# Performance work log

Measured on AMD Instinct MI355X. Metric: run time of the kernel, lower is better.

Reference implementation:

```python
import jax, jax.numpy as jnp
import numpy as np

N_WIRES = 12
BLOCK_CONFIGS = [(12, 3), (12, 3)]
HAM_OFFSET = 0.0
HAM_COEFF = 1.0
BATCH = 4096


def _sq(psi, w):
    # view statevector (B, 2^n) as (B, left, 2, right) isolating wire w
    B = psi.shape[0]
    n = N_WIRES
    return psi.reshape(B, 1 << w, 2, 1 << (n - 1 - w))


def _rx(psi, theta, w):
    s = _sq(psi, w)
    t = jnp.asarray(theta, jnp.float32).reshape(-1, 1, 1, 1) * 0.5
    out = jnp.cos(t) * s - 1j * jnp.sin(t) * jnp.flip(s, axis=2)
    return out.reshape(psi.shape)


def _ry(psi, theta, w):
    # [[c,-s],[s,c]]: new = cos*psi + sin*sgn*flip(psi), sgn = (-1, +1)
    s = _sq(psi, w)
    t = jnp.asarray(theta, jnp.float32).reshape(-1, 1, 1, 1) * 0.5
    sgn = jnp.array([-1.0, 1.0], jnp.float32).reshape(1, 1, 2, 1)
    out = jnp.cos(t) * s + jnp.sin(t) * sgn * jnp.flip(s, axis=2)
    return out.reshape(psi.shape)


def _rz(psi, theta, w):
    # diag(e^{-i t/2}, e^{+i t/2})
    s = _sq(psi, w)
    t = jnp.asarray(theta, jnp.float32).reshape(-1, 1, 1, 1) * 0.5
    z = jnp.array([-1.0, 1.0], jnp.float32).reshape(1, 1, 2, 1)
    out = s * jnp.exp(1j * (t * z).astype(jnp.complex64))
    return out.reshape(psi.shape)


def _cnot(psi, c, t):
    B = psi.shape[0]
    n = N_WIRES
    lo, hi = (c, t) if c < t else (t, c)
    s = psi.reshape(B, 1 << lo, 2, 1 << (hi - lo - 1), 2, 1 << (n - 1 - hi))
    ctrl_ax = 2 if c == lo else 4
    tgt_ax = 4 if c == lo else 2
    p0 = jax.lax.index_in_dim(s, 0, axis=ctrl_ax, keepdims=True)
    p1 = jnp.flip(jax.lax.index_in_dim(s, 1, axis=ctrl_ax, keepdims=True), axis=tgt_ax)
    out = jnp.concatenate([p0, p1], axis=ctrl_ax)
    return out.reshape(psi.shape)


def setup_inputs() -> dict:
    key = jax.random.key(0)
    k1, k2 = jax.random.split(key)
    total_encode = sum(ne for ne, _ in BLOCK_CONFIGS)
    total_ansatz = sum(ld for _, ld in BLOCK_CONFIGS)
    x = jax.random.normal(k1, (BATCH, total_encode), dtype=jnp.float32)
    ansatz_weights = jax.random.uniform(
        k2, (total_ansatz, 3, N_WIRES), dtype=jnp.float32,
        minval=-np.pi, maxval=np.pi)
    return {"x": x, "ansatz_weights": ansatz_weights}


def reference(x, ansatz_weights):
    B = x.shape[0]
    n = N_WIRES
    psi = jnp.zeros((B, 1 << n), jnp.complex64).at[:, 0].set(1.0)
    param_col = 0
    ansatz_block = 0
    for n_encode, linear_depth in BLOCK_CONFIGS:
        for j in range(n_encode):
            wire = j % n
            if param_col < x.shape[1]:
                psi = _rx(psi, x[:, param_col], wire)
            param_col += 1
        for _ in range(linear_depth):
            w = ansatz_weights[ansatz_block]
            for i in range(n):
                psi = _ry(psi, w[0, i], i)
                psi = _rz(psi, w[1, i], i)
                psi = _ry(psi, w[2, i], i)
            for i in range(n):
                psi = _cnot(psi, i, (i + 1) % n)
            ansatz_block += 1
    # <H> with H = offset + coeff * sum_i Z_i : diagonal = n - 2*popcount(k)
    probs = psi.real ** 2 + psi.imag ** 2
    k = jnp.arange(1 << n)
    pop = ((k[:, None] >> jnp.arange(n)[None, :]) & 1).sum(-1).astype(jnp.float32)
    diag = HAM_OFFSET + HAM_COEFF * (n - 2.0 * pop)
    expval = probs @ diag  # (B,)
    return expval[:, None]
```

## Files before the change

### kernel.cpp

```cpp
#include <hip/hip_runtime.h>
#include <math.h>

#define NT 256
#define NS 4096

typedef float f32x2 __attribute__((ext_vector_type(2)));

constexpr int ring_pi_c(int k) {
    int u = k ^ (k >> 1);
    u ^= u >> 2; u ^= u >> 4; u ^= u >> 8;
    int w0 = ((u >> 11) ^ u) & 1;
    return (u & 0x7FF) | (w0 << 11);
}
constexpr int sig2(int m) { return m ^ ((m >> 4) & 0xF) ^ ((m >> 8) & 0xF); }

__device__ __forceinline__ void app1p(f32x2 ab, f32x2 cd, f32x2& a0, f32x2& a1) {
    f32x2 n0, n1;
    asm("v_pk_mul_f32 %0, %2, %4 op_sel:[0,0] op_sel_hi:[1,0]\n\t"
        "v_pk_fma_f32 %0, %2, %4, %0 op_sel:[1,1,0] op_sel_hi:[0,1,1] neg_hi:[0,1,0]\n\t"
        "v_pk_fma_f32 %0, %3, %5, %0 op_sel:[0,0,0] op_sel_hi:[1,0,1] neg_lo:[0,1,0] neg_hi:[0,1,0]\n\t"
        "v_pk_fma_f32 %0, %3, %5, %0 op_sel:[1,1,0] op_sel_hi:[0,1,1] neg_lo:[0,1,0]\n\t"
        "v_pk_mul_f32 %1, %3, %4 op_sel:[0,0] op_sel_hi:[1,0]\n\t"
        "v_pk_fma_f32 %1, %3, %4, %1 op_sel:[1,1,0] op_sel_hi:[0,1,1] neg_lo:[0,1,0]\n\t"
        "v_pk_fma_f32 %1, %2, %5, %1 op_sel:[0,0,0] op_sel_hi:[1,0,1]\n\t"
        "v_pk_fma_f32 %1, %2, %5, %1 op_sel:[1,1,0] op_sel_hi:[0,1,1] neg_lo:[0,1,0]"
        : "=&v"(n0), "=&v"(n1)
        : "v"(a0), "v"(a1), "v"(ab), "v"(cd));
    a0 = n0; a1 = n1;
}

template<int P>
__device__ __forceinline__ void gate_on_bit(f32x2 a[16], f32x2 ab, f32x2 cd) {
    #pragma unroll
    for (int r = 0; r < 16; ++r)
        if (!(r & (1 << P)))
            app1p(ab, cd, a[r], a[r | (1 << P)]);
}

__device__ __forceinline__ void load_gate(const float4* __restrict__ Uw,
                                          const float2* __restrict__ cs12,
                                          int l, int w, bool fold,
                                          f32x2& ab, f32x2& cd) {
    float4 g = Uw[l * 12 + w];
    float A = g.x, B = g.y, C = g.z, D = g.w;
    if (fold) {
        float2 sc = cs12[w];
        float c = sc.x, s = sc.y;
        float A2 = A*c + D*s, B2 = B*c - C*s, C2 = C*c + B*s, D2 = D*c - A*s;
        A = A2; B = B2; C = C2; D = D2;
    }
    ab = f32x2{A, B}; cd = f32x2{C, D};
}

__global__ void prep_kernel(const float* __restrict__ x,
                            const float* __restrict__ wts,
                            float4* __restrict__ Uw,
                            float2* __restrict__ cs,
                            int total)
{
    int idx = blockIdx.x * blockDim.x + threadIdx.x;
    if (idx < total) {
        float th = 0.5f * x[idx];
        float s, c; sincosf(th, &s, &c);
        cs[idx] = make_float2(c, s);
    }
    if (idx < 72) {
        int ab = idx / 12, w = idx % 12;
        float a  = 0.5f * wts[(ab * 3 + 0) * 12 + w];
        float bb = 0.5f * wts[(ab * 3 + 1) * 12 + w];
        float g  = 0.5f * wts[(ab * 3 + 2) * 12 + w];
        float sa, ca, sb, cb, sg, cg;
        sincosf(a,  &sa, &ca);
        sincosf(bb, &sb, &cb);
        sincosf(g,  &sg, &cg);
        float A = cb * (ca * cg - sa * sg);
        float B = sb * (ca * cg + sa * sg);
        float C = cb * (sa * cg + ca * sg);
        float D = sb * (sa * cg - ca * sg);
        Uw[idx] = make_float4(A, B, C, D);
    }
}

__global__ __launch_bounds__(NT, 2)
void tqhea_kernel(const float4* __restrict__ Uw,
                  const float2* __restrict__ cs,
                  float* __restrict__ out)
{
    __shared__ f32x2 psi[NS];

    const int b = blockIdx.x;
    const int t = threadIdx.x;

    const int lo = t & 0xF, h = t >> 4;
    const int tb     = (t & 0xF0) | (lo ^ h);
    const int baseP1 = (h << 8) | (lo ^ h);
    const int baseP2 = (t << 4) | (lo ^ h);
    const int Qt     = sig2(ring_pi_c(t << 4));
    const int Pt     = ring_pi_c(t << 4);

    const float2* csb  = cs + b * 24;
    const float2* cs12 = csb + 12;

    {
        float2 rc[12];
        #pragma unroll
        for (int i = 0; i < 12; ++i) rc[i] = csb[i];
        float mlo = 1.f;
        #pragma unroll
        for (int bit = 0; bit < 8; ++bit)
            mlo *= ((t >> bit) & 1) ? rc[11 - bit].y : rc[11 - bit].x;
        int pct = __popc(t);
        #pragma unroll
        for (int r = 0; r < 16; ++r) {
            float mhi = 1.f;
            #pragma unroll
            for (int p = 0; p < 4; ++p)
                mhi *= ((r >> p) & 1) ? rc[3 - p].y : rc[3 - p].x;
            float mag = mhi * mlo;
            int pc = (pct + __popc(r)) & 3;
            f32x2 v;
            v.x = (pc == 0) ? mag : ((pc == 2) ? -mag : 0.f);
            v.y = (pc == 1) ? -mag : ((pc == 3) ? mag : 0.f);
            psi[(r << 8) | (tb ^ r)] = v;
        }
    }
    __syncthreads();

    float acc = 0.f;

    #pragma unroll 1
    for (int l = 0; l < 6; ++l) {
        const bool fold = (l == 3);
        f32x2 a[16];
        f32x2 gab, gcd;

        #pragma unroll
        for (int r = 0; r < 16; ++r) a[r] = psi[(r << 8) | (tb ^ r)];
        load_gate(Uw, cs12, l, 0, fold, gab, gcd); gate_on_bit<3>(a, gab, gcd);
        load_gate(Uw, cs12, l, 1, fold, gab, gcd); gate_on_bit<2>(a, gab, gcd);
        load_gate(Uw, cs12, l, 2, fold, gab, gcd); gate_on_bit<1>(a, gab, gcd);
        load_gate(Uw, cs12, l, 3, fold, gab, gcd); gate_on_bit<0>(a, gab, gcd);
        #pragma unroll
        for (int r = 0; r < 16; ++r) psi[(r << 8) | (tb ^ r)] = a[r];
        __syncthreads();

        #pragma unroll
        for (int r = 0; r < 16; ++r) a[r] = psi[baseP1 ^ (17 * r)];
        load_gate(Uw, cs12, l, 4, fold, gab, gcd); gate_on_bit<3>(a, gab, gcd);
        load_gate(Uw, cs12, l, 5, fold, gab, gcd); gate_on_bit<2>(a, gab, gcd);
        load_gate(Uw, cs12, l, 6, fold, gab, gcd); gate_on_bit<1>(a, gab, gcd);
        load_gate(Uw, cs12, l, 7, fold, gab, gcd); gate_on_bit<0>(a, gab, gcd);
        #pragma unroll
        for (int r = 0; r < 16; ++r) psi[baseP1 ^ (17 * r)] = a[r];
        __syncthreads();

        #pragma unroll
        for (int r = 0; r < 16; ++r) a[r] = psi[baseP2 ^ r];
        if (l < 5) __syncthreads();
        load_gate(Uw, cs12, l, 8,  fold, gab, gcd); gate_on_bit<3>(a, gab, gcd);
        load_gate(Uw, cs12, l, 9,  fold, gab, gcd); gate_on_bit<2>(a, gab, gcd);
        load_gate(Uw, cs12, l, 10, fold, gab, gcd); gate_on_bit<1>(a, gab, gcd);
        load_gate(Uw, cs12, l, 11, fold, gab, gcd); gate_on_bit<0>(a, gab, gcd);
        if (l < 5) {
            #pragma unroll
            for (int r = 0; r < 16; ++r)
                psi[Qt ^ sig2(ring_pi_c(r))] = a[r];
            __syncthreads();
        } else {
            #pragma unroll
            for (int r = 0; r < 16; ++r) {
                float d = 12.0f - 2.0f * (float)__popc(Pt ^ ring_pi_c(r));
                acc += (a[r].x * a[r].x + a[r].y * a[r].y) * d;
            }
        }
    }

    #pragma unroll
    for (int off = 32; off > 0; off >>= 1)
        acc += __shfl_down(acc, off);
    __syncthreads();
    if ((t & 63) == 0) ((float*)psi)[t >> 6] = acc;
    __syncthreads();
    if (t == 0) {
        const float* rb = (const float*)psi;
        out[b] = rb[0] + rb[1] + rb[2] + rb[3];
    }
}

extern "C" void kernel_launch(void* const* d_in, const int* in_sizes, int n_in,
                              void* d_out, int out_size, void* d_ws, size_t ws_size,
                              hipStream_t stream) {
    const float* x   = (const float*)d_in[0];
    const float* wts = (const float*)d_in[1];
    float* out = (float*)d_out;
    int B = in_sizes[0] / 24;

    float4* Uw = (float4*)d_ws;
    float2* cs = (float2*)((char*)d_ws + 1152);
    int total = B * 24;

    prep_kernel<<<dim3((total + NT - 1) / NT), dim3(NT), 0, stream>>>(x, wts, Uw, cs, total);
    tqhea_kernel<<<dim3(B), dim3(NT), 0, stream>>>(Uw, cs, out);
}
```

Measured before the change: 215.4 us.

## Simulate each statevector with one 64-lane wavefront holding 64 amplitudes per lane

The batch kernel now uses a single 64-thread wavefront per sample instead of 256 threads. Each lane keeps 64 complex amplitudes in registers, so six gates are applied per register pass and only two LDS transposes are needed per layer instead of three. The initial encoded state is built directly in registers, and the final reduction becomes a single wave shuffle. In exchange, register pressure rises sharply (128 floats of state per lane), which risks spills, and the number of waves per CU drops.

```diff
diff --git a/kernel.cpp b/kernel.cpp
--- a/kernel.cpp
+++ b/kernel.cpp
@@ -1,7 +1,8 @@
 #include <hip/hip_runtime.h>
 #include <math.h>
 
-#define NT 256
+#define NTP 256
+#define NT 64
 #define NS 4096
 
 typedef float f32x2 __attribute__((ext_vector_type(2)));
@@ -12,7 +13,11 @@
     int w0 = ((u >> 11) ^ u) & 1;
     return (u & 0x7FF) | (w0 << 11);
 }
-constexpr int sig2(int m) { return m ^ ((m >> 4) & 0xF) ^ ((m >> 8) & 0xF); }
+constexpr int gfun(int n) {
+    int n0 = n & 1, n1 = (n >> 1) & 1, n2 = (n >> 2) & 1, n3 = (n >> 3) & 1;
+    return (n1) | ((n0 ^ n1 ^ n2) << 1) | ((n0 ^ n2 ^ n3) << 2) | ((n0 ^ n3) << 3);
+}
+constexpr int sigf(int k) { return k ^ gfun((k >> 6) & 15); }
 
 __device__ __forceinline__ void app1p(f32x2 ab, f32x2 cd, f32x2& a0, f32x2& a1) {
     f32x2 n0, n1;
@@ -30,18 +35,18 @@
 }
 
 template<int P>
-__device__ __forceinline__ void gate_on_bit(f32x2 a[16], f32x2 ab, f32x2 cd) {
+__device__ __forceinline__ void gate_on_bit6(f32x2 a[64], f32x2 ab, f32x2 cd) {
     #pragma unroll
-    for (int r = 0; r < 16; ++r)
+    for (int r = 0; r < 64; ++r)
         if (!(r & (1 << P)))
             app1p(ab, cd, a[r], a[r | (1 << P)]);
 }
 
 __device__ __forceinline__ void load_gate(const float4* __restrict__ Uw,
                                           const float2* __restrict__ cs12,
-                                          int l, int w, bool fold,
+                                          int lay, int w, bool fold,
                                           f32x2& ab, f32x2& cd) {
-    float4 g = Uw[l * 12 + w];
+    float4 g = Uw[lay * 12 + w];
     float A = g.x, B = g.y, C = g.z, D = g.w;
     if (fold) {
         float2 sc = cs12[w];
@@ -81,95 +86,97 @@
     }
 }
 
-__global__ __launch_bounds__(NT, 2)
+__global__ __launch_bounds__(NT, 1)
 void tqhea_kernel(const float4* __restrict__ Uw,
                   const float2* __restrict__ cs,
                   float* __restrict__ out)
 {
     __shared__ f32x2 psi[NS];
 
-    const int b = blockIdx.x;
-    const int t = threadIdx.x;
-
-    const int lo = t & 0xF, h = t >> 4;
-    const int tb     = (t & 0xF0) | (lo ^ h);
-    const int baseP1 = (h << 8) | (lo ^ h);
-    const int baseP2 = (t << 4) | (lo ^ h);
-    const int Qt     = sig2(ring_pi_c(t << 4));
-    const int Pt     = ring_pi_c(t << 4);
+    const int b  = blockIdx.x;
+    const int ln = threadIdx.x;
 
     const float2* csb  = cs + b * 24;
     const float2* cs12 = csb + 12;
 
+    f32x2 a[64];
+
     {
         float2 rc[12];
         #pragma unroll
         for (int i = 0; i < 12; ++i) rc[i] = csb[i];
-        float mlo = 1.f;
-        #pragma unroll
-        for (int bit = 0; bit < 8; ++bit)
-            mlo *= ((t >> bit) & 1) ? rc[11 - bit].y : rc[11 - bit].x;
-        int pct = __popc(t);
-        #pragma unroll
-        for (int r = 0; r < 16; ++r) {
-            float mhi = 1.f;
+        float mlan = 1.f;
+        #pragma unroll
+        for (int bit = 0; bit < 6; ++bit)
+            mlan *= ((ln >> bit) & 1) ? rc[11 - bit].y : rc[11 - bit].x;
+        int q = __popc(ln) & 3;
+        float pre = (q == 0) ? mlan : (q == 2) ? -mlan : 0.f;
+        float pim = (q == 1) ? -mlan : (q == 3) ? mlan : 0.f;
+        float mA[8], mB[8];
+        #pragma unroll
+        for (int i = 0; i < 8; ++i) {
+            mA[i] = (((i>>2)&1)?rc[0].y:rc[0].x) * (((i>>1)&1)?rc[1].y:rc[1].x) * ((i&1)?rc[2].y:rc[2].x);
+            mB[i] = (((i>>2)&1)?rc[3].y:rc[3].x) * (((i>>1)&1)?rc[4].y:rc[4].x) * ((i&1)?rc[5].y:rc[5].x);
+        }
+        #pragma unroll
+        for (int r = 0; r < 64; ++r) {
+            float m = mA[r >> 3] * mB[r & 7];
+            const int rot = __popc(r) & 3;
+            float vx, vy;
+            if (rot == 0)      { vx =  pre * m; vy =  pim * m; }
+            else if (rot == 1) { vx =  pim * m; vy = -pre * m; }
+            else if (rot == 2) { vx = -pre * m; vy = -pim * m; }
+            else               { vx = -pim * m; vy =  pre * m; }
+            a[r] = f32x2{vx, vy};
+        }
+    }
+
+    const int gl    = gfun(ln & 15);
+    const int baseB = (ln << 6) | gl;
+    const int baseR = sigf(ring_pi_c(ln << 6));
+    const int Pl    = ring_pi_c(ln << 6);
+
+    float acc = 0.f;
+
+    #pragma unroll 1
+    for (int lay = 0; lay < 6; ++lay) {
+        const bool fold = (lay == 3);
+        f32x2 gab, gcd;
+
+        load_gate(Uw, cs12, lay, 0, fold, gab, gcd); gate_on_bit6<5>(a, gab, gcd);
+        load_gate(Uw, cs12, lay, 1, fold, gab, gcd); gate_on_bit6<4>(a, gab, gcd);
+        load_gate(Uw, cs12, lay, 2, fold, gab, gcd); gate_on_bit6<3>(a, gab, gcd);
+        load_gate(Uw, cs12, lay, 3, fold, gab, gcd); gate_on_bit6<2>(a, gab, gcd);
+        load_gate(Uw, cs12, lay, 4, fold, gab, gcd); gate_on_bit6<1>(a, gab, gcd);
+        load_gate(Uw, cs12, lay, 5, fold, gab, gcd); gate_on_bit6<0>(a, gab, gcd);
+
+        #pragma unroll
+        for (int r = 0; r < 64; ++r)
+            psi[(r << 6) | (ln ^ gfun(r & 15))] = a[r];
+        __syncthreads();
+        #pragma unroll
+        for (int r = 0; r < 64; ++r)
+            a[r] = psi[(baseB ^ (r & 15)) | (r & 48)];
+
+        load_gate(Uw, cs12, lay, 6,  fold, gab, gcd); gate_on_bit6<5>(a, gab, gcd);
+        load_gate(Uw, cs12, lay, 7,  fold, gab, gcd); gate_on_bit6<4>(a, gab, gcd);
+        load_gate(Uw, cs12, lay, 8,  fold, gab, gcd); gate_on_bit6<3>(a, gab, gcd);
+        load_gate(Uw, cs12, lay, 9,  fold, gab, gcd); gate_on_bit6<2>(a, gab, gcd);
+        load_gate(Uw, cs12, lay, 10, fold, gab, gcd); gate_on_bit6<1>(a, gab, gcd);
+        load_gate(Uw, cs12, lay, 11, fold, gab, gcd); gate_on_bit6<0>(a, gab, gcd);
+
+        if (lay < 5) {
             #pragma unroll
-            for (int p = 0; p < 4; ++p)
-                mhi *= ((r >> p) & 1) ? rc[3 - p].y : rc[3 - p].x;
-            float mag = mhi * mlo;
-            int pc = (pct + __popc(r)) & 3;
-            f32x2 v;
-            v.x = (pc == 0) ? mag : ((pc == 2) ? -mag : 0.f);
-            v.y = (pc == 1) ? -mag : ((pc == 3) ? mag : 0.f);
-            psi[(r << 8) | (tb ^ r)] = v;
-        }
-    }
-    __syncthreads();
-
-    float acc = 0.f;
-
-    #pragma unroll 1
-    for (int l = 0; l < 6; ++l) {
-        const bool fold = (l == 3);
-        f32x2 a[16];
-        f32x2 gab, gcd;
-
-        #pragma unroll
-        for (int r = 0; r < 16; ++r) a[r] = psi[(r << 8) | (tb ^ r)];
-        load_gate(Uw, cs12, l, 0, fold, gab, gcd); gate_on_bit<3>(a, gab, gcd);
-        load_gate(Uw, cs12, l, 1, fold, gab, gcd); gate_on_bit<2>(a, gab, gcd);
-        load_gate(Uw, cs12, l, 2, fold, gab, gcd); gate_on_bit<1>(a, gab, gcd);
-        load_gate(Uw, cs12, l, 3, fold, gab, gcd); gate_on_bit<0>(a, gab, gcd);
-        #pragma unroll
-        for (int r = 0; r < 16; ++r) psi[(r << 8) | (tb ^ r)] = a[r];
-        __syncthreads();
-
-        #pragma unroll
-        for (int r = 0; r < 16; ++r) a[r] = psi[baseP1 ^ (17 * r)];
-        load_gate(Uw, cs12, l, 4, fold, gab, gcd); gate_on_bit<3>(a, gab, gcd);
-        load_gate(Uw, cs12, l, 5, fold, gab, gcd); gate_on_bit<2>(a, gab, gcd);
-        load_gate(Uw, cs12, l, 6, fold, gab, gcd); gate_on_bit<1>(a, gab, gcd);
-        load_gate(Uw, cs12, l, 7, fold, gab, gcd); gate_on_bit<0>(a, gab, gcd);
-        #pragma unroll
-        for (int r = 0; r < 16; ++r) psi[baseP1 ^ (17 * r)] = a[r];
-        __syncthreads();
-
-        #pragma unroll
-        for (int r = 0; r < 16; ++r) a[r] = psi[baseP2 ^ r];
-        if (l < 5) __syncthreads();
-        load_gate(Uw, cs12, l, 8,  fold, gab, gcd); gate_on_bit<3>(a, gab, gcd);
-        load_gate(Uw, cs12, l, 9,  fold, gab, gcd); gate_on_bit<2>(a, gab, gcd);
-        load_gate(Uw, cs12, l, 10, fold, gab, gcd); gate_on_bit<1>(a, gab, gcd);
-        load_gate(Uw, cs12, l, 11, fold, gab, gcd); gate_on_bit<0>(a, gab, gcd);
-        if (l < 5) {
+            for (int r = 0; r < 64; ++r)
+                psi[baseR ^ sigf(ring_pi_c(r))] = a[r];
+            __syncthreads();
             #pragma unroll
-            for (int r = 0; r < 16; ++r)
-                psi[Qt ^ sig2(ring_pi_c(r))] = a[r];
-            __syncthreads();
+            for (int r = 0; r < 64; ++r)
+                a[r] = psi[(r << 6) | (ln ^ gfun(r & 15))];
         } else {
             #pragma unroll
-            for (int r = 0; r < 16; ++r) {
-                float d = 12.0f - 2.0f * (float)__popc(Pt ^ ring_pi_c(r));
+            for (int r = 0; r < 64; ++r) {
+                float d = 12.0f - 2.0f * (float)__popc(Pl ^ ring_pi_c(r));
                 acc += (a[r].x * a[r].x + a[r].y * a[r].y) * d;
             }
         }
@@ -178,13 +185,7 @@
     #pragma unroll
     for (int off = 32; off > 0; off >>= 1)
         acc += __shfl_down(acc, off);
-    __syncthreads();
-    if ((t & 63) == 0) ((float*)psi)[t >> 6] = acc;
-    __syncthreads();
-    if (t == 0) {
-        const float* rb = (const float*)psi;
-        out[b] = rb[0] + rb[1] + rb[2] + rb[3];
-    }
+    if (ln == 0) out[b] = acc;
 }
 
 extern "C" void kernel_launch(void* const* d_in, const int* in_sizes, int n_in,
@@ -199,6 +200,6 @@
     float2* cs = (float2*)((char*)d_ws + 1152);
     int total = B * 24;
 
-    prep_kernel<<<dim3((total + NT - 1) / NT), dim3(NT), 0, stream>>>(x, wts, Uw, cs, total);
+    prep_kernel<<<dim3((total + NTP - 1) / NTP), dim3(NTP), 0, stream>>>(x, wts, Uw, cs, total);
     tqhea_kernel<<<dim3(B), dim3(NT), 0, stream>>>(Uw, cs, out);
 }
```

Result: slower. 224.3 us (+4.2%).

## Decompose gates into real Y rotations plus precomputed diagonal phase tables

Applied to the files above, without the earlier changes.

Each fused single-qubit unitary is split into a real Y-rotation and Z phases. The Z phases are commuted through the CNOT ring and collected into per-layer diagonal phase tables, computed once by a new prep kernel and applied as one complex multiply per amplitude. The per-gate butterfly drops from eight packed FMAs to four, and the fold of the second encoding block becomes a separate X-layer pass. In exchange there is an extra layer pass, a 7x4096 table read from global memory by every block, one more kernel launch, and atan2-based phase extraction that may cost accuracy.

```diff
diff --git a/kernel.cpp b/kernel.cpp
--- a/kernel.cpp
+++ b/kernel.cpp
@@ -1,6 +1,7 @@
 #include <hip/hip_runtime.h>
 #include <math.h>
 
+#define NTP 256
 #define NT 256
 #define NS 4096
 
@@ -12,51 +13,48 @@
     int w0 = ((u >> 11) ^ u) & 1;
     return (u & 0x7FF) | (w0 << 11);
 }
+constexpr int ring_sigma_c(int k) {
+    int s = (k ^ (k >> 1)) & 0x3FF;
+    int b10 = ((k >> 10) ^ (k >> 11) ^ k) & 1;
+    int b11 = ((k >> 11) ^ k) & 1;
+    return s | (b10 << 10) | (b11 << 11);
+}
 constexpr int sig2(int m) { return m ^ ((m >> 4) & 0xF) ^ ((m >> 8) & 0xF); }
 
-__device__ __forceinline__ void app1p(f32x2 ab, f32x2 cd, f32x2& a0, f32x2& a1) {
+__device__ __forceinline__ void ygate(f32x2 cs_, f32x2& a0, f32x2& a1) {
     f32x2 n0, n1;
-    asm("v_pk_mul_f32 %0, %2, %4 op_sel:[0,0] op_sel_hi:[1,0]\n\t"
-        "v_pk_fma_f32 %0, %2, %4, %0 op_sel:[1,1,0] op_sel_hi:[0,1,1] neg_hi:[0,1,0]\n\t"
-        "v_pk_fma_f32 %0, %3, %5, %0 op_sel:[0,0,0] op_sel_hi:[1,0,1] neg_lo:[0,1,0] neg_hi:[0,1,0]\n\t"
-        "v_pk_fma_f32 %0, %3, %5, %0 op_sel:[1,1,0] op_sel_hi:[0,1,1] neg_lo:[0,1,0]\n\t"
-        "v_pk_mul_f32 %1, %3, %4 op_sel:[0,0] op_sel_hi:[1,0]\n\t"
-        "v_pk_fma_f32 %1, %3, %4, %1 op_sel:[1,1,0] op_sel_hi:[0,1,1] neg_lo:[0,1,0]\n\t"
-        "v_pk_fma_f32 %1, %2, %5, %1 op_sel:[0,0,0] op_sel_hi:[1,0,1]\n\t"
-        "v_pk_fma_f32 %1, %2, %5, %1 op_sel:[1,1,0] op_sel_hi:[0,1,1] neg_lo:[0,1,0]"
+    asm("v_pk_mul_f32 %0, %3, %4 op_sel:[0,1] op_sel_hi:[1,1] neg_lo:[0,1] neg_hi:[0,1]\n\t"
+        "v_pk_fma_f32 %0, %2, %4, %0 op_sel:[0,0,0] op_sel_hi:[1,0,1]\n\t"
+        "v_pk_mul_f32 %1, %2, %4 op_sel:[0,1] op_sel_hi:[1,1]\n\t"
+        "v_pk_fma_f32 %1, %3, %4, %1 op_sel:[0,0,0] op_sel_hi:[1,0,1]"
         : "=&v"(n0), "=&v"(n1)
-        : "v"(a0), "v"(a1), "v"(ab), "v"(cd));
+        : "v"(a0), "v"(a1), "v"(cs_));
     a0 = n0; a1 = n1;
 }
 
+__device__ __forceinline__ void cdiag(f32x2 e, f32x2& a) {
+    f32x2 m;
+    asm("v_pk_mul_f32 %0, %1, %2 op_sel:[1,1] op_sel_hi:[0,1] neg_lo:[1,0]\n\t"
+        "v_pk_fma_f32 %0, %1, %2, %0 op_sel:[0,0,0] op_sel_hi:[1,0,1]"
+        : "=&v"(m) : "v"(a), "v"(e));
+    a = m;
+}
+
 template<int P>
-__device__ __forceinline__ void gate_on_bit(f32x2 a[16], f32x2 ab, f32x2 cd) {
+__device__ __forceinline__ void ygate_on_bit(f32x2 a[16], float2 cs_) {
+    f32x2 v = f32x2{cs_.x, cs_.y};
     #pragma unroll
     for (int r = 0; r < 16; ++r)
         if (!(r & (1 << P)))
-            app1p(ab, cd, a[r], a[r | (1 << P)]);
-}
-
-__device__ __forceinline__ void load_gate(const float4* __restrict__ Uw,
-                                          const float2* __restrict__ cs12,
-                                          int l, int w, bool fold,
-                                          f32x2& ab, f32x2& cd) {
-    float4 g = Uw[l * 12 + w];
-    float A = g.x, B = g.y, C = g.z, D = g.w;
-    if (fold) {
-        float2 sc = cs12[w];
-        float c = sc.x, s = sc.y;
-        float A2 = A*c + D*s, B2 = B*c - C*s, C2 = C*c + B*s, D2 = D*c - A*s;
-        A = A2; B = B2; C = C2; D = D2;
-    }
-    ab = f32x2{A, B}; cd = f32x2{C, D};
-}
-
-__global__ void prep_kernel(const float* __restrict__ x,
-                            const float* __restrict__ wts,
-                            float4* __restrict__ Uw,
-                            float2* __restrict__ cs,
-                            int total)
+            ygate(v, a[r], a[r | (1 << P)]);
+}
+
+__global__ void prep1_kernel(const float* __restrict__ x,
+                             const float* __restrict__ wts,
+                             float2* __restrict__ ys,
+                             float2* __restrict__ cdah,
+                             float2* __restrict__ cs,
+                             int total)
 {
     int idx = blockIdx.x * blockDim.x + threadIdx.x;
     if (idx < total) {
@@ -77,13 +75,45 @@
         float B = sb * (ca * cg + sa * sg);
         float C = cb * (sa * cg + ca * sg);
         float D = sb * (sa * cg - ca * sg);
-        Uw[idx] = make_float4(A, B, C, D);
-    }
+        float cy = sqrtf(A * A + B * B);
+        float sy = sqrtf(C * C + D * D);
+        float f00 = atan2f(-B, A);
+        float f10 = atan2f(D, C);
+        ys[idx]   = make_float2(cy, sy);
+        cdah[idx] = make_float2(0.5f * (f10 - f00), -0.5f * (f10 + f00));
+    }
+}
+
+__global__ void prep2_kernel(const float2* __restrict__ cdah,
+                             float2* __restrict__ tabs)
+{
+    int idx = blockIdx.x * blockDim.x + threadIdx.x;
+    if (idx >= 7 * NS) return;
+    int tl = idx >> 12, k = idx & (NS - 1);
+    int sk = ring_sigma_c(k);
+    const float QP = 0.7853981633974483f;
+    float ph = 0.f;
+    for (int w = 0; w < 12; ++w) {
+        float zd = ((k  >> (11 - w)) & 1) ? 1.f : -1.f;
+        float zc = ((sk >> (11 - w)) & 1) ? 1.f : -1.f;
+        float dcf, ccf;
+        if (tl == 3)      { dcf = QP;                       ccf = cdah[2 * 12 + w].x; }
+        else if (tl == 4) { dcf = cdah[3 * 12 + w].y - QP;  ccf = 0.f; }
+        else {
+            int ald = (tl < 3) ? tl : tl - 1;
+            dcf = cdah[ald * 12 + w].y;
+            ccf = (tl == 0) ? 0.f : cdah[((tl < 3) ? tl - 1 : tl - 2) * 12 + w].x;
+        }
+        ph += zd * dcf + zc * ccf;
+    }
+    float s, c; sincosf(ph, &s, &c);
+    tabs[idx] = make_float2(c, s);
 }
 
 __global__ __launch_bounds__(NT, 2)
-void tqhea_kernel(const float4* __restrict__ Uw,
+void tqhea_kernel(const float2* __restrict__ ys,
                   const float2* __restrict__ cs,
+                  const f32x2*  __restrict__ tabs,
                   float* __restrict__ out)
 {
     __shared__ f32x2 psi[NS];
@@ -129,49 +159,58 @@
     float acc = 0.f;
 
     #pragma unroll 1
-    for (int l = 0; l < 6; ++l) {
-        const bool fold = (l == 3);
+    for (int lay = 0; lay < 7; ++lay) {
+        const bool isx = (lay == 3);
+        const float2* yrow = isx ? cs12 : ys + ((lay < 3) ? lay : lay - 1) * 12;
+        const f32x2* Tl = tabs + lay * NS;
         f32x2 a[16];
-        f32x2 gab, gcd;
-
+
+        f32x2 e[16];
+        #pragma unroll
+        for (int r = 0; r < 16; ++r) e[r] = Tl[(r << 8) | t];
         #pragma unroll
         for (int r = 0; r < 16; ++r) a[r] = psi[(r << 8) | (tb ^ r)];
-        load_gate(Uw, cs12, l, 0, fold, gab, gcd); gate_on_bit<3>(a, gab, gcd);
-        load_gate(Uw, cs12, l, 1, fold, gab, gcd); gate_on_bit<2>(a, gab, gcd);
-        load_gate(Uw, cs12, l, 2, fold, gab, gcd); gate_on_bit<1>(a, gab, gcd);
-        load_gate(Uw, cs12, l, 3, fold, gab, gcd); gate_on_bit<0>(a, gab, gcd);
+        #pragma unroll
+        for (int r = 0; r < 16; ++r) cdiag(e[r], a[r]);
+        ygate_on_bit<3>(a, yrow[0]);
+        ygate_on_bit<2>(a, yrow[1]);
+        ygate_on_bit<1>(a, yrow[2]);
+        ygate_on_bit<0>(a, yrow[3]);
         #pragma unroll
         for (int r = 0; r < 16; ++r) psi[(r << 8) | (tb ^ r)] = a[r];
         __syncthreads();
 
         #pragma unroll
         for (int r = 0; r < 16; ++r) a[r] = psi[baseP1 ^ (17 * r)];
-        load_gate(Uw, cs12, l, 4, fold, gab, gcd); gate_on_bit<3>(a, gab, gcd);
-        load_gate(Uw, cs12, l, 5, fold, gab, gcd); gate_on_bit<2>(a, gab, gcd);
-        load_gate(Uw, cs12, l, 6, fold, gab, gcd); gate_on_bit<1>(a, gab, gcd);
-        load_gate(Uw, cs12, l, 7, fold, gab, gcd); gate_on_bit<0>(a, gab, gcd);
+        ygate_on_bit<3>(a, yrow[4]);
+        ygate_on_bit<2>(a, yrow[5]);
+        ygate_on_bit<1>(a, yrow[6]);
+        ygate_on_bit<0>(a, yrow[7]);
         #pragma unroll
         for (int r = 0; r < 16; ++r) psi[baseP1 ^ (17 * r)] = a[r];
         __syncthreads();
 
         #pragma unroll
         for (int r = 0; r < 16; ++r) a[r] = psi[baseP2 ^ r];
-        if (l < 5) __syncthreads();
-        load_gate(Uw, cs12, l, 8,  fold, gab, gcd); gate_on_bit<3>(a, gab, gcd);
-        load_gate(Uw, cs12, l, 9,  fold, gab, gcd); gate_on_bit<2>(a, gab, gcd);
-        load_gate(Uw, cs12, l, 10, fold, gab, gcd); gate_on_bit<1>(a, gab, gcd);
-        load_gate(Uw, cs12, l, 11, fold, gab, gcd); gate_on_bit<0>(a, gab, gcd);
-        if (l < 5) {
-            #pragma unroll
-            for (int r = 0; r < 16; ++r)
-                psi[Qt ^ sig2(ring_pi_c(r))] = a[r];
-            __syncthreads();
-        } else {
+        if (lay < 6 && !isx) __syncthreads();
+        ygate_on_bit<3>(a, yrow[8]);
+        ygate_on_bit<2>(a, yrow[9]);
+        ygate_on_bit<1>(a, yrow[10]);
+        ygate_on_bit<0>(a, yrow[11]);
+        if (lay == 6) {
             #pragma unroll
             for (int r = 0; r < 16; ++r) {
                 float d = 12.0f - 2.0f * (float)__popc(Pt ^ ring_pi_c(r));
                 acc += (a[r].x * a[r].x + a[r].y * a[r].y) * d;
             }
+        } else if (isx) {
+            #pragma unroll
+            for (int r = 0; r < 16; ++r) psi[baseP2 ^ r] = a[r];
+            __syncthreads();
+        } else {
+            #pragma unroll
+            for (int r = 0; r < 16; ++r) psi[Qt ^ sig2(ring_pi_c(r))] = a[r];
+            __syncthreads();
         }
     }
 
@@ -194,11 +233,15 @@
     const float* wts = (const float*)d_in[1];
     float* out = (float*)d_out;
     int B = in_sizes[0] / 24;
-
-    float4* Uw = (float4*)d_ws;
-    float2* cs = (float2*)((char*)d_ws + 1152);
     int total = B * 24;
 
-    prep_kernel<<<dim3((total + NT - 1) / NT), dim3(NT), 0, stream>>>(x, wts, Uw, cs, total);
-    tqhea_kernel<<<dim3(B), dim3(NT), 0, stream>>>(Uw, cs, out);
-}
+    char* ws = (char*)d_ws;
+    float2* ys   = (float2*)(ws);
+    float2* cdah = (float2*)(ws + 576);
+    float2* cs   = (float2*)(ws + 1152);
+    float2* tabs = (float2*)(ws + 1152 + (size_t)total * 8);
+
+    prep1_kernel<<<dim3((total + NTP - 1) / NTP), dim3(NTP), 0, stream>>>(x, wts, ys, cdah, cs, total);
+    prep2_kernel<<<dim3((7 * NS + NTP - 1) / NTP), dim3(NTP), 0, stream>>>(cdah, tabs);
+    tqhea_kernel<<<dim3(B), dim3(NT), 0, stream>>>(ys, cs, (const f32x2*)tabs, out);
+}
```

Result: faster. 202.2 us (-6.1%).
